# Kernel optimization log

Measured on AMD Instinct MI355X. Metric: run time of the kernel, lower is better.

The kernel has to match this reference:

```python
import jax, jax.numpy as jnp
import numpy as np

H = 1024
NH = 16
HD = H // NH

def setup_inputs() -> dict:
    key = jax.random.key(0)
    ks = jax.random.split(key, 8)
    s = 1.0 / np.sqrt(H)
    hidden_states = jax.random.normal(ks[0], (2, 2048, H), dtype=jnp.float32)
    attention_mask = jnp.zeros((2, 1, 1, 2048), dtype=jnp.float32)
    Wq = jax.random.uniform(ks[1], (H, H), jnp.float32, -s, s)
    bq = jax.random.uniform(ks[2], (H,), jnp.float32, -s, s)
    Wk = jax.random.uniform(ks[3], (H, H), jnp.float32, -s, s)
    bk = jax.random.uniform(ks[4], (H,), jnp.float32, -s, s)
    Wv = jax.random.uniform(ks[5], (H, H), jnp.float32, -s, s)
    bv = jax.random.uniform(ks[6], (H,), jnp.float32, -s, s)
    return {"hidden_states": hidden_states, "attention_mask": attention_mask,
            "Wq": Wq, "bq": bq, "Wk": Wk, "bk": bk, "Wv": Wv, "bv": bv}

def _split_heads(x):
    B, L, _ = x.shape
    return x.reshape(B, L, NH, HD).transpose(0, 2, 1, 3)  # [B, nh, L, hd]

def reference(hidden_states, attention_mask, Wq, bq, Wk, bk, Wv, bv):
    # QKV projections (nn.Linear: x @ W.T + b)
    Q = _split_heads(hidden_states @ Wq.T + bq)
    K = _split_heads(hidden_states @ Wk.T + bk)
    V = _split_heads(hidden_states @ Wv.T + bv)
    scale = 1.0 / np.sqrt(HD)
    scores = jnp.einsum('bhqd,bhkd->bhqk', Q, K) * scale  # [B, nh, L, L]
    scores = scores + attention_mask
    probs = jax.nn.softmax(scores, axis=-1)  # dropout in eval mode = identity
    context = jnp.einsum('bhqk,bhkd->bhqd', probs, V)
    B, _, L, _ = context.shape
    return context.transpose(0, 2, 1, 3).reshape(B, L, H)
```

## Files before the change

kernel.cpp:

```cpp
#include <hip/hip_runtime.h>
#include <math.h>
#include <stdint.h>

#define H_DIM 1024
#define NH 16
#define HD 64
#define B_DIM 2
#define L_DIM 2048
#define M_TOT (B_DIM * L_DIM)

typedef __bf16 bf16_t;
typedef __bf16 bf16x8 __attribute__((ext_vector_type(8)));
typedef __bf16 bf16x4 __attribute__((ext_vector_type(4)));
typedef float  f32x4  __attribute__((ext_vector_type(4)));

#define AS1 const __attribute__((address_space(1))) void*
#define AS3 __attribute__((address_space(3))) void*

__global__ __launch_bounds__(256)
void cast_all(const float* __restrict__ x,
              const float* __restrict__ Wq, const float* __restrict__ Wk,
              const float* __restrict__ Wv, bf16_t* __restrict__ dst)
{
    const size_t idx = ((size_t)blockIdx.x * 256 + threadIdx.x) * 4;
    const float* src;
    size_t off;
    if (idx < (size_t)M_TOT * H_DIM) { src = x; off = idx; }
    else {
        size_t j = idx - (size_t)M_TOT * H_DIM;
        int z = (int)(j >> 20);
        off = j & ((1u << 20) - 1);
        src = (z == 0) ? Wq : (z == 1) ? Wk : Wv;
    }
    const float4 v = *(const float4*)(src + off);
    bf16x4 o;
    o[0] = (bf16_t)v.x; o[1] = (bf16_t)v.y;
    o[2] = (bf16_t)v.z; o[3] = (bf16_t)v.w;
    *(bf16x4*)(dst + idx) = o;
}

__global__ __launch_bounds__(256, 1)
void qkv_mfma(const bf16_t* __restrict__ xb, const bf16_t* __restrict__ wb,
              const float* __restrict__ bq, const float* __restrict__ bk,
              const float* __restrict__ bv,
              bf16_t* __restrict__ qb, bf16_t* __restrict__ kb,
              bf16_t* __restrict__ vt)
{
    __shared__ bf16_t As0[128 * 32];
    __shared__ bf16_t As1[128 * 32];
    __shared__ bf16_t As2[128 * 32];
    __shared__ bf16_t Bs0[3][128 * 32];
    __shared__ bf16_t Bs1[3][128 * 32];
    __shared__ bf16_t Bs2[3][128 * 32];

    const int tid = threadIdx.x;
    const int n   = blockIdx.x;
    const int bn  = (n & 7) * 128;
    const int bm  = (n >> 3) * 128;

    const int wave = tid >> 6;
    const int lane = tid & 63;
    const int lc   = lane & 15;
    const int quad = lane >> 4;
    const int wm   = wave >> 1;
    const int wn   = wave & 1;

    f32x4 acc[3][4][4];
    #pragma unroll
    for (int z = 0; z < 3; ++z)
        #pragma unroll
        for (int i = 0; i < 4; ++i)
            #pragma unroll
            for (int j = 0; j < 4; ++j)
                acc[z][i][j] = (f32x4){0.f, 0.f, 0.f, 0.f};

    const int srow = tid >> 2;
    const int sseg = tid & 3;
    const bf16_t* gA = xb + (size_t)(bm + srow) * H_DIM + (sseg ^ (srow & 3)) * 8;
    const bf16_t* gB = wb + (size_t)(bn + srow) * H_DIM + (sseg ^ (srow & 3)) * 8;
    const int woff = wave * 1024;

    auto stage = [&](int k0, bf16_t* A_, bf16_t (*B_)[128 * 32]) {
        __builtin_amdgcn_global_load_lds((AS1)(gA + k0),
            (AS3)((char*)A_ + woff), 16, 0, 0);
        __builtin_amdgcn_global_load_lds((AS1)(gA + k0 + (size_t)64 * H_DIM),
            (AS3)((char*)A_ + woff + 4096), 16, 0, 0);
        #pragma unroll
        for (int z = 0; z < 3; ++z) {
            const bf16_t* g = gB + (size_t)z * H_DIM * H_DIM + k0;
            __builtin_amdgcn_global_load_lds((AS1)(g),
                (AS3)((char*)B_[z] + woff), 16, 0, 0);
            __builtin_amdgcn_global_load_lds((AS1)(g + (size_t)64 * H_DIM),
                (AS3)((char*)B_[z] + woff + 4096), 16, 0, 0);
        }
    };

    const int slot = (quad ^ (lc & 3)) * 8;
    auto compute = [&](const bf16_t* A_, const bf16_t (*B_)[128 * 32]) {
        bf16x8 a[4];
        #pragma unroll
        for (int mi = 0; mi < 4; ++mi)
            a[mi] = *(const bf16x8*)(A_ + (wm * 64 + mi * 16 + lc) * 32 + slot);
        #pragma unroll
        for (int z = 0; z < 3; ++z) {
            bf16x8 b[4];
            #pragma unroll
            for (int ni = 0; ni < 4; ++ni)
                b[ni] = *(const bf16x8*)(B_[z] + (wn * 64 + ni * 16 + lc) * 32 + slot);
            #pragma unroll
            for (int mi = 0; mi < 4; ++mi)
                #pragma unroll
                for (int ni = 0; ni < 4; ++ni)
                    acc[z][mi][ni] = __builtin_amdgcn_mfma_f32_16x16x32_bf16(
                        a[mi], b[ni], acc[z][mi][ni], 0, 0, 0);
        }
    };

    auto step = [&](int kk, bf16_t* cA, bf16_t (*cB)[128 * 32],
                    bf16_t* nA, bf16_t (*nB)[128 * 32], bool doStage) {
        __builtin_amdgcn_s_waitcnt(0x0F78);
        __builtin_amdgcn_s_barrier();
        if (doStage) stage((kk + 2) * 32, nA, nB);
        compute(cA, cB);
    };

    stage(0,  As0, Bs0);
    stage(32, As1, Bs1);
    #pragma unroll 1
    for (int t = 0; t < 10; ++t) {
        const int kk = t * 3;
        step(kk,     As0, Bs0, As2, Bs2, true);
        step(kk + 1, As1, Bs1, As0, Bs0, true);
        step(kk + 2, As2, Bs2, As1, Bs1, true);
    }
    step(30, As0, Bs0, As2, Bs2, false);
    __builtin_amdgcn_s_waitcnt(0x0F70);
    __builtin_amdgcn_s_barrier();
    compute(As1, Bs1);

    const int nb = bn + wn * 64;
    #pragma unroll
    for (int z = 0; z < 3; ++z) {
        const float* bias = (z == 0) ? bq : (z == 1) ? bk : bv;
        float biasv[4];
        #pragma unroll
        for (int ni = 0; ni < 4; ++ni) biasv[ni] = bias[nb + ni * 16 + lc];

        #pragma unroll
        for (int mi = 0; mi < 4; ++mi) {
            const int m0 = bm + wm * 64 + mi * 16 + quad * 4;
            if (z == 2) {
                const int b_ = m0 >> 11;
                const int l0 = m0 & 2047;
                #pragma unroll
                for (int ni = 0; ni < 4; ++ni) {
                    const int nn = nb + ni * 16 + lc;
                    const int h = nn >> 6, d = nn & 63;
                    bf16x4 pk;
                    #pragma unroll
                    for (int r = 0; r < 4; ++r)
                        pk[r] = (bf16_t)(acc[z][mi][ni][r] + biasv[ni]);
                    *(bf16x4*)(vt + (((size_t)(b_ * NH + h)) * HD + d) * L_DIM + l0) = pk;
                }
            } else {
                bf16_t* dst = (z == 0) ? qb : kb;
                #pragma unroll
                for (int r = 0; r < 4; ++r) {
                    const int m  = m0 + r;
                    const int b_ = m >> 11;
                    const int l  = m & 2047;
                    #pragma unroll
                    for (int ni = 0; ni < 4; ++ni) {
                        const int nn = nb + ni * 16 + lc;
                        const int h = nn >> 6, d = nn & 63;
                        dst[(((size_t)(b_ * NH + h)) * L_DIM + l) * HD + d] =
                            (bf16_t)(acc[z][mi][ni][r] + biasv[ni]);
                    }
                }
            }
        }
    }
}

#define EXP_C   0.180336879f
#define LOG2E   1.442695041f
#define EXP_SH  11.541560327f

__device__ __forceinline__ void attn_tile32(
    int kbase, bool pre,
    const bf16_t* curK, const bf16_t* curV,
    bf16_t* nxtK, bf16_t* nxtV,
    const bf16_t* gKw, const bf16_t* gVw, int wo,
    bf16_t* Ps, const float* mvsL, int lc, int quad,
    const bf16x8 (&bQ)[2][2], f32x4 (&o)[2][4], float (&rs)[2])
{
    __builtin_amdgcn_s_waitcnt(0x0F70);
    __builtin_amdgcn_s_barrier();

    const int e = lc & 7;

    bf16x8 kf[2][2];
    #pragma unroll
    for (int ni = 0; ni < 2; ++ni) {
        const bf16_t* p = curK + (ni * 16 + lc) * 64;
        kf[ni][0] = *(const bf16x8*)(p + ((quad ^ e) << 3));
        kf[ni][1] = *(const bf16x8*)(p + (((quad ^ e) ^ 4) << 3));
    }

    if (pre) {
        const int nk = kbase + 32;
        __builtin_amdgcn_global_load_lds(
            (AS1)(gKw + (size_t)nk * 64),
            (AS3)(nxtK + wo), 16, 0, 0);
        __builtin_amdgcn_global_load_lds(
            (AS1)(gVw + nk),
            (AS3)(nxtV + wo), 16, 0, 0);
    }

    f32x4 mvs[2];
    #pragma unroll
    for (int ni = 0; ni < 2; ++ni)
        mvs[ni] = *(const f32x4*)(mvsL + kbase + ni * 16 + quad * 4);

    #pragma unroll
    for (int f = 0; f < 2; ++f) {
        f32x4 s[2];
        __builtin_amdgcn_s_setprio(1);
        #pragma unroll
        for (int ni = 0; ni < 2; ++ni) {
            f32x4 t = (f32x4){0.f, 0.f, 0.f, 0.f};
            t = __builtin_amdgcn_mfma_f32_16x16x32_bf16(kf[ni][0], bQ[f][0], t, 0, 0, 0);
            t = __builtin_amdgcn_mfma_f32_16x16x32_bf16(kf[ni][1], bQ[f][1], t, 0, 0, 0);
            s[ni] = t;
        }
        __builtin_amdgcn_s_setprio(0);
        float acc = 0.f;
        #pragma unroll
        for (int ni = 0; ni < 2; ++ni) {
            bf16x4 pk;
            #pragma unroll
            for (int r = 0; r < 4; ++r) {
                const float p = __builtin_amdgcn_exp2f(s[ni][r] * EXP_C + mvs[ni][r]);
                acc += p;
                pk[r] = (bf16_t)p;
            }
            const int c = f * 4 + ni * 2 + (quad >> 1);
            *(bf16x4*)(Ps + lc * 64 + ((c ^ e) << 3) + ((quad & 1) << 2)) = pk;
        }
        rs[f] += acc;
    }

    bf16x8 vf[4];
    const int e2 = lc >> 1;
    #pragma unroll
    for (int dg = 0; dg < 4; ++dg) {
        const int p  = dg * 8 + (lc >> 1);
        const int ch = (((lc & 1) << 2) + quad) ^ e2;
        vf[dg] = *(const bf16x8*)(curV + p * 64 + (ch << 3));
    }

    #pragma unroll
    for (int f = 0; f < 2; ++f) {
        const int c = f * 4 + quad;
        const bf16x8 bP = *(const bf16x8*)(Ps + lc * 64 + ((c ^ e) << 3));
        __builtin_amdgcn_s_setprio(1);
        #pragma unroll
        for (int dg = 0; dg < 4; ++dg)
            o[f][dg] = __builtin_amdgcn_mfma_f32_16x16x32_bf16(vf[dg], bP, o[f][dg], 0, 0, 0);
        __builtin_amdgcn_s_setprio(0);
    }
}

__global__ __launch_bounds__(256, 4)
void attn_mfma(const bf16_t* __restrict__ qb, const bf16_t* __restrict__ kb,
               const bf16_t* __restrict__ vt, const float* __restrict__ mask,
               float* __restrict__ out, float* __restrict__ o1,
               float* __restrict__ l0, float* __restrict__ l1)
{
    __shared__ bf16_t Ks0[32 * 64];
    __shared__ bf16_t Ks1[32 * 64];
    __shared__ bf16_t Vs0[32 * 64];
    __shared__ bf16_t Vs1[32 * 64];
    __shared__ bf16_t Ps[4][16 * 64];
    __shared__ float  Ms[1024];

    const int tid  = threadIdx.x;
    const int wave = tid >> 6;
    const int lane = tid & 63;
    const int lc   = lane & 15;
    const int quad = lane >> 4;
    const int rl   = lane >> 3;
    const int sg   = lane & 7;

    const int n    = blockIdx.x;
    const int bh   = (n & 7) * 4 + ((n >> 3) & 3);
    const int q0   = ((n >> 5) & 15) * 128 + wave * 32;
    const int ks   = (n >> 9) & 1;
    const int k0   = ks << 10;
    const int b_   = bh >> 4;
    const int h    = bh & 15;

    bf16_t* Psw = Ps[wave];

    bf16x8 bQ[2][2];
    #pragma unroll
    for (int f = 0; f < 2; ++f) {
        const bf16_t* Qp = qb + ((size_t)bh * L_DIM + q0 + f * 16 + lc) * HD + quad * 8;
        bQ[f][0] = *(const bf16x8*)(Qp);
        bQ[f][1] = *(const bf16x8*)(Qp + 32);
    }

    const bf16_t* Kbase = kb + (size_t)bh * L_DIM * HD;
    const bf16_t* Vbase = vt + (size_t)bh * HD * L_DIM;
    const float*  mrow  = mask + (size_t)b_ * L_DIM + k0;

    {
        const float4 m4 = *(const float4*)(mrow + tid * 4);
        f32x4 w;
        w[0] = m4.x * LOG2E - EXP_SH;
        w[1] = m4.y * LOG2E - EXP_SH;
        w[2] = m4.z * LOG2E - EXP_SH;
        w[3] = m4.w * LOG2E - EXP_SH;
        *(f32x4*)(Ms + tid * 4) = w;
    }

    const int cV = sg ^ rl;
    const bf16_t* gKw = Kbase + (size_t)(k0 + wave * 8 + rl) * 64 + (sg ^ rl) * 8;
    const bf16_t* gVw = Vbase + k0
                      + (size_t)(wave * 16 + rl * 2 + (cV >> 2)) * L_DIM
                      + (cV & 3) * 8;
    const int wo = wave * 512;

    f32x4 o[2][4];
    #pragma unroll
    for (int f = 0; f < 2; ++f)
        #pragma unroll
        for (int dg = 0; dg < 4; ++dg) o[f][dg] = (f32x4){0.f, 0.f, 0.f, 0.f};
    float rs[2] = {0.f, 0.f};

    __builtin_amdgcn_global_load_lds((AS1)(gKw), (AS3)(Ks0 + wo), 16, 0, 0);
    __builtin_amdgcn_global_load_lds((AS1)(gVw), (AS3)(Vs0 + wo), 16, 0, 0);

    __syncthreads();

    #pragma unroll 1
    for (int t2 = 0; t2 < 16; ++t2) {
        const int kb0 = t2 * 64;
        attn_tile32(kb0,      true,     Ks0, Vs0, Ks1, Vs1, gKw, gVw, wo, Psw,
                    Ms, lc, quad, bQ, o, rs);
        attn_tile32(kb0 + 32, t2 < 15,  Ks1, Vs1, Ks0, Vs0, gKw, gVw, wo, Psw,
                    Ms, lc, quad, bQ, o, rs);
    }

    float* obase = (ks == 0) ? out : o1;
    float* lbase = (ks == 0) ? l0  : l1;
    #pragma unroll
    for (int f = 0; f < 2; ++f) {
        float l = rs[f];
        l += __shfl_xor(l, 16);
        l += __shfl_xor(l, 32);
        if (quad == 0)
            lbase[(size_t)bh * L_DIM + q0 + f * 16 + lc] = l;
        float* orow = obase + ((size_t)(b_ * L_DIM + q0 + f * 16 + lc)) * H_DIM
                    + h * HD + quad * 4;
        #pragma unroll
        for (int dg = 0; dg < 4; ++dg)
            *(f32x4*)(orow + dg * 16) = o[f][dg];
    }
}

__global__ __launch_bounds__(256)
void attn_combine(const float* __restrict__ o1,
                  const float* __restrict__ l0, const float* __restrict__ l1,
                  float* __restrict__ out)
{
    const size_t idx = ((size_t)blockIdx.x * 256 + threadIdx.x) * 8;
    const int m   = (int)(idx >> 10);
    const int col = (int)(idx & 1023);
    const int b_  = m >> 11;
    const int q   = m & 2047;
    const int h   = col >> 6;
    const size_t lidx = ((size_t)(b_ * NH + h)) * L_DIM + q;
    const float inv = 1.0f / (l0[lidx] + l1[lidx]);
    f32x4 a0 = *(const f32x4*)(out + idx);
    f32x4 a1 = *(const f32x4*)(out + idx + 4);
    const f32x4 b0 = *(const f32x4*)(o1 + idx);
    const f32x4 b1 = *(const f32x4*)(o1 + idx + 4);
    a0 = (a0 + b0) * inv;
    a1 = (a1 + b1) * inv;
    *(f32x4*)(out + idx)     = a0;
    *(f32x4*)(out + idx + 4) = a1;
}

extern "C" void kernel_launch(void* const* d_in, const int* in_sizes, int n_in,
                              void* d_out, int out_size, void* d_ws, size_t ws_size,
                              hipStream_t stream) {
    const float* hidden = (const float*)d_in[0];
    const float* mask   = (const float*)d_in[1];
    const float* Wq     = (const float*)d_in[2];
    const float* bq     = (const float*)d_in[3];
    const float* Wk     = (const float*)d_in[4];
    const float* bk     = (const float*)d_in[5];
    const float* Wv     = (const float*)d_in[6];
    const float* bv     = (const float*)d_in[7];
    float* out = (float*)d_out;

    const size_t XN = (size_t)M_TOT * H_DIM;
    const size_t WN = (size_t)3 * H_DIM * H_DIM;
    bf16_t* xwb = (bf16_t*)d_ws;
    bf16_t* qb  = xwb + XN + WN;
    bf16_t* kb  = qb + XN;
    bf16_t* vt  = kb + XN;
    float*  o1  = (float*)(vt + XN);
    float*  l0  = o1 + XN;
    float*  l1  = l0 + (size_t)B_DIM * NH * L_DIM;

    cast_all<<<(int)((XN + WN) / 1024), 256, 0, stream>>>(hidden, Wq, Wk, Wv, xwb);

    qkv_mfma<<<256, 256, 0, stream>>>(xwb, xwb + XN, bq, bk, bv, qb, kb, vt);

    attn_mfma<<<1024, 256, 0, stream>>>(qb, kb, vt, mask, out, o1, l0, l1);

    attn_combine<<<2048, 256, 0, stream>>>(o1, l0, l1, out);
}
```

Before: 171.7 us.

## Split fused QKV GEMM into separate blocks per projection for occupancy

The QKV projection kernel now launches 768 blocks, each computing one of Q, K or V for a 128x128 tile, instead of 256 blocks that each computed all three. This cuts per-block accumulators and LDS by about a third, and launch bounds are raised to allow three blocks per CU. The waitcnt is adjusted for the smaller number of outstanding loads per stage. The cost is that each activation tile is loaded three times instead of once, which adds global/L2 traffic in exchange for more parallelism and latency hiding.

```diff
diff --git a/kernel.cpp b/kernel.cpp
--- a/kernel.cpp
+++ b/kernel.cpp
@@ -39,7 +39,7 @@
     *(bf16x4*)(dst + idx) = o;
 }
 
-__global__ __launch_bounds__(256, 1)
+__global__ __launch_bounds__(256, 3)
 void qkv_mfma(const bf16_t* __restrict__ xb, const bf16_t* __restrict__ wb,
               const float* __restrict__ bq, const float* __restrict__ bk,
               const float* __restrict__ bv,
@@ -49,12 +49,14 @@
     __shared__ bf16_t As0[128 * 32];
     __shared__ bf16_t As1[128 * 32];
     __shared__ bf16_t As2[128 * 32];
-    __shared__ bf16_t Bs0[3][128 * 32];
-    __shared__ bf16_t Bs1[3][128 * 32];
-    __shared__ bf16_t Bs2[3][128 * 32];
+    __shared__ bf16_t Bs0[128 * 32];
+    __shared__ bf16_t Bs1[128 * 32];
+    __shared__ bf16_t Bs2[128 * 32];
 
     const int tid = threadIdx.x;
-    const int n   = blockIdx.x;
+    const int n0  = blockIdx.x;
+    const int z   = n0 >> 8;
+    const int n   = n0 & 255;
     const int bn  = (n & 7) * 128;
     const int bm  = (n >> 3) * 128;
 
@@ -65,60 +67,52 @@
     const int wm   = wave >> 1;
     const int wn   = wave & 1;
 
-    f32x4 acc[3][4][4];
-    #pragma unroll
-    for (int z = 0; z < 3; ++z)
-        #pragma unroll
-        for (int i = 0; i < 4; ++i)
-            #pragma unroll
-            for (int j = 0; j < 4; ++j)
-                acc[z][i][j] = (f32x4){0.f, 0.f, 0.f, 0.f};
+    f32x4 acc[4][4];
+    #pragma unroll
+    for (int i = 0; i < 4; ++i)
+        #pragma unroll
+        for (int j = 0; j < 4; ++j)
+            acc[i][j] = (f32x4){0.f, 0.f, 0.f, 0.f};
 
     const int srow = tid >> 2;
     const int sseg = tid & 3;
     const bf16_t* gA = xb + (size_t)(bm + srow) * H_DIM + (sseg ^ (srow & 3)) * 8;
-    const bf16_t* gB = wb + (size_t)(bn + srow) * H_DIM + (sseg ^ (srow & 3)) * 8;
+    const bf16_t* gB = wb + (size_t)z * H_DIM * H_DIM
+                     + (size_t)(bn + srow) * H_DIM + (sseg ^ (srow & 3)) * 8;
     const int woff = wave * 1024;
 
-    auto stage = [&](int k0, bf16_t* A_, bf16_t (*B_)[128 * 32]) {
+    auto stage = [&](int k0, bf16_t* A_, bf16_t* B_) {
         __builtin_amdgcn_global_load_lds((AS1)(gA + k0),
             (AS3)((char*)A_ + woff), 16, 0, 0);
         __builtin_amdgcn_global_load_lds((AS1)(gA + k0 + (size_t)64 * H_DIM),
             (AS3)((char*)A_ + woff + 4096), 16, 0, 0);
-        #pragma unroll
-        for (int z = 0; z < 3; ++z) {
-            const bf16_t* g = gB + (size_t)z * H_DIM * H_DIM + k0;
-            __builtin_amdgcn_global_load_lds((AS1)(g),
-                (AS3)((char*)B_[z] + woff), 16, 0, 0);
-            __builtin_amdgcn_global_load_lds((AS1)(g + (size_t)64 * H_DIM),
-                (AS3)((char*)B_[z] + woff + 4096), 16, 0, 0);
-        }
+        __builtin_amdgcn_global_load_lds((AS1)(gB + k0),
+            (AS3)((char*)B_ + woff), 16, 0, 0);
+        __builtin_amdgcn_global_load_lds((AS1)(gB + k0 + (size_t)64 * H_DIM),
+            (AS3)((char*)B_ + woff + 4096), 16, 0, 0);
     };
 
     const int slot = (quad ^ (lc & 3)) * 8;
-    auto compute = [&](const bf16_t* A_, const bf16_t (*B_)[128 * 32]) {
+    auto compute = [&](const bf16_t* A_, const bf16_t* B_) {
         bf16x8 a[4];
         #pragma unroll
         for (int mi = 0; mi < 4; ++mi)
             a[mi] = *(const bf16x8*)(A_ + (wm * 64 + mi * 16 + lc) * 32 + slot);
-        #pragma unroll
-        for (int z = 0; z < 3; ++z) {
-            bf16x8 b[4];
+        bf16x8 b[4];
+        #pragma unroll
+        for (int ni = 0; ni < 4; ++ni)
+            b[ni] = *(const bf16x8*)(B_ + (wn * 64 + ni * 16 + lc) * 32 + slot);
+        #pragma unroll
+        for (int mi = 0; mi < 4; ++mi)
             #pragma unroll
             for (int ni = 0; ni < 4; ++ni)
-                b[ni] = *(const bf16x8*)(B_[z] + (wn * 64 + ni * 16 + lc) * 32 + slot);
-            #pragma unroll
-            for (int mi = 0; mi < 4; ++mi)
-                #pragma unroll
-                for (int ni = 0; ni < 4; ++ni)
-                    acc[z][mi][ni] = __builtin_amdgcn_mfma_f32_16x16x32_bf16(
-                        a[mi], b[ni], acc[z][mi][ni], 0, 0, 0);
-        }
+                acc[mi][ni] = __builtin_amdgcn_mfma_f32_16x16x32_bf16(
+                    a[mi], b[ni], acc[mi][ni], 0, 0, 0);
     };
 
-    auto step = [&](int kk, bf16_t* cA, bf16_t (*cB)[128 * 32],
-                    bf16_t* nA, bf16_t (*nB)[128 * 32], bool doStage) {
-        __builtin_amdgcn_s_waitcnt(0x0F78);
+    auto step = [&](int kk, bf16_t* cA, bf16_t* cB,
+                    bf16_t* nA, bf16_t* nB, bool doStage) {
+        __builtin_amdgcn_s_waitcnt(0x0F74);
         __builtin_amdgcn_s_barrier();
         if (doStage) stage((kk + 2) * 32, nA, nB);
         compute(cA, cB);
@@ -139,43 +133,40 @@
     compute(As1, Bs1);
 
     const int nb = bn + wn * 64;
-    #pragma unroll
-    for (int z = 0; z < 3; ++z) {
-        const float* bias = (z == 0) ? bq : (z == 1) ? bk : bv;
-        float biasv[4];
-        #pragma unroll
-        for (int ni = 0; ni < 4; ++ni) biasv[ni] = bias[nb + ni * 16 + lc];
-
-        #pragma unroll
-        for (int mi = 0; mi < 4; ++mi) {
-            const int m0 = bm + wm * 64 + mi * 16 + quad * 4;
-            if (z == 2) {
-                const int b_ = m0 >> 11;
-                const int l0 = m0 & 2047;
+    const float* bias = (z == 0) ? bq : (z == 1) ? bk : bv;
+    float biasv[4];
+    #pragma unroll
+    for (int ni = 0; ni < 4; ++ni) biasv[ni] = bias[nb + ni * 16 + lc];
+
+    #pragma unroll
+    for (int mi = 0; mi < 4; ++mi) {
+        const int m0 = bm + wm * 64 + mi * 16 + quad * 4;
+        if (z == 2) {
+            const int b_ = m0 >> 11;
+            const int l0 = m0 & 2047;
+            #pragma unroll
+            for (int ni = 0; ni < 4; ++ni) {
+                const int nn = nb + ni * 16 + lc;
+                const int h = nn >> 6, d = nn & 63;
+                bf16x4 pk;
+                #pragma unroll
+                for (int r = 0; r < 4; ++r)
+                    pk[r] = (bf16_t)(acc[mi][ni][r] + biasv[ni]);
+                *(bf16x4*)(vt + (((size_t)(b_ * NH + h)) * HD + d) * L_DIM + l0) = pk;
+            }
+        } else {
+            bf16_t* dst = (z == 0) ? qb : kb;
+            #pragma unroll
+            for (int r = 0; r < 4; ++r) {
+                const int m  = m0 + r;
+                const int b_ = m >> 11;
+                const int l  = m & 2047;
                 #pragma unroll
                 for (int ni = 0; ni < 4; ++ni) {
                     const int nn = nb + ni * 16 + lc;
                     const int h = nn >> 6, d = nn & 63;
-                    bf16x4 pk;
-                    #pragma unroll
-                    for (int r = 0; r < 4; ++r)
-                        pk[r] = (bf16_t)(acc[z][mi][ni][r] + biasv[ni]);
-                    *(bf16x4*)(vt + (((size_t)(b_ * NH + h)) * HD + d) * L_DIM + l0) = pk;
-                }
-            } else {
-                bf16_t* dst = (z == 0) ? qb : kb;
-                #pragma unroll
-                for (int r = 0; r < 4; ++r) {
-                    const int m  = m0 + r;
-                    const int b_ = m >> 11;
-                    const int l  = m & 2047;
-                    #pragma unroll
-                    for (int ni = 0; ni < 4; ++ni) {
-                        const int nn = nb + ni * 16 + lc;
-                        const int h = nn >> 6, d = nn & 63;
-                        dst[(((size_t)(b_ * NH + h)) * L_DIM + l) * HD + d] =
-                            (bf16_t)(acc[z][mi][ni][r] + biasv[ni]);
-                    }
+                    dst[(((size_t)(b_ * NH + h)) * L_DIM + l) * HD + d] =
+                        (bf16_t)(acc[mi][ni][r] + biasv[ni]);
                 }
             }
         }
@@ -417,7 +408,7 @@
 
     cast_all<<<(int)((XN + WN) / 1024), 256, 0, stream>>>(hidden, Wq, Wk, Wv, xwb);
 
-    qkv_mfma<<<256, 256, 0, stream>>>(xwb, xwb + XN, bq, bk, bv, qb, kb, vt);
+    qkv_mfma<<<768, 256, 0, stream>>>(xwb, xwb + XN, bq, bk, bv, qb, kb, vt);
 
     attn_mfma<<<1024, 256, 0, stream>>>(qb, kb, vt, mask, out, o1, l0, l1);
 
```

New measurement: 178.8 us. 4.2% more time.
